# Kernel optimization log

Measured on AMD Instinct MI355X. Metric: run time of the kernel, lower is better.

## Reference

```python
import jax, jax.numpy as jnp
import numpy as np
import math

B, IN_CH, IMG = 32, 3, 128
D, L, H, MLP, P = 512, 8, 8, 2048, 8
HD = D // H
EPS = 1e-5


def _conv(x, w, b, stride, pad):
    y = jax.lax.conv_general_dilated(x, w, (stride, stride), pad,
                                     dimension_numbers=("NCHW", "OIHW", "NCHW"))
    return y + b[None, :, None, None]


def _gn(x, g, b, groups):
    Bn, C, Hh, W = x.shape
    xr = x.reshape(Bn, groups, C // groups, Hh, W)
    m = jnp.mean(xr, axis=(2, 3, 4), keepdims=True)
    v = jnp.var(xr, axis=(2, 3, 4), keepdims=True)
    xr = (xr - m) / jnp.sqrt(v + EPS)
    return xr.reshape(Bn, C, Hh, W) * g[None, :, None, None] + b[None, :, None, None]


def _ln(x, g, b):
    m = jnp.mean(x, axis=-1, keepdims=True)
    v = jnp.var(x, axis=-1, keepdims=True)
    return (x - m) / jnp.sqrt(v + EPS) * g + b


def _rot_half(x):
    # interleaved pairs: (x0,x1) -> (-x1,x0)
    x1, x2 = x[..., 0::2], x[..., 1::2]
    return jnp.stack((-x2, x1), axis=-1).reshape(x.shape)


def _xpos_tables(n_pos, hd):
    # faithful to rotary_embedding_torch with use_xpos=True, scale_base=512
    inv = 1.0 / (10000.0 ** (jnp.arange(0, hd, 2, dtype=jnp.float32) / hd))
    seq = jnp.arange(n_pos, dtype=jnp.float32)
    freqs = jnp.repeat(seq[:, None] * inv[None, :], 2, axis=-1)  # (n_pos, hd) interleaved
    sv = (jnp.arange(0, hd, 2, dtype=jnp.float32) + 0.4 * hd) / (1.4 * hd)
    power = (seq - n_pos // 2) / 512.0
    scale = sv[None, :] ** power[:, None]                        # (n_pos, hd//2)
    scale = jnp.concatenate([scale, scale], axis=-1)             # library uses cat, not interleave
    return jnp.cos(freqs), jnp.sin(freqs), scale


def _pos2d(N, Dd):
    g = int(math.isqrt(N))
    y = jnp.tile(jnp.arange(g), g).astype(jnp.float32)
    x = jnp.repeat(jnp.arange(g), g).astype(jnp.float32)
    dq = Dd // 4
    omega = jnp.exp(jnp.arange(dq, dtype=jnp.float32) * -(math.log(10000.0) / dq))
    px, py = x[:, None] * omega, y[:, None] * omega
    return jnp.concatenate([jnp.sin(px), jnp.cos(px), jnp.sin(py), jnp.cos(py)], axis=-1)[None]


def setup_inputs() -> dict:
    key = jax.random.key(0)
    ks = iter(jax.random.split(key, 40))
    def rn(shape, s=0.02):
        return jax.random.normal(next(ks), shape, jnp.float32) * s
    return dict(
        x=jax.random.normal(next(ks), (B, IN_CH, IMG, IMG), jnp.float32),
        conv1_w=rn((32, 3, 3, 3)), conv1_b=jnp.zeros((32,), jnp.float32),
        gn1_g=jnp.ones((32,), jnp.float32), gn1_b=jnp.zeros((32,), jnp.float32),
        conv2_w=rn((64, 32, 3, 3)), conv2_b=jnp.zeros((64,), jnp.float32),
        gn2_g=jnp.ones((64,), jnp.float32), gn2_b=jnp.zeros((64,), jnp.float32),
        patch_w=rn((D, 64, P, P)), patch_b=jnp.zeros((D,), jnp.float32),
        cls_token=rn((1, 1, D), 1.0),
        ln1_g=jnp.ones((L, D), jnp.float32), ln1_b=jnp.zeros((L, D), jnp.float32),
        qkv_w=rn((L, D, 3 * D)), qkv_b=jnp.zeros((L, 3 * D), jnp.float32),
        out_w=rn((L, D, D)), out_b=jnp.zeros((L, D), jnp.float32),
        ln2_g=jnp.ones((L, D), jnp.float32), ln2_b=jnp.zeros((L, D), jnp.float32),
        w1_w=rn((L, D, MLP)), w1_b=jnp.zeros((L, MLP), jnp.float32),
        w2_w=rn((L, D, MLP)), w2_b=jnp.zeros((L, MLP), jnp.float32),
        w3_w=rn((L, MLP, D)), w3_b=jnp.zeros((L, D), jnp.float32),
        fn_g=jnp.ones((D,), jnp.float32), fn_b=jnp.zeros((D,), jnp.float32),
    )


def _forward(x, conv1_w, conv1_b, gn1_g, gn1_b, conv2_w, conv2_b, gn2_g, gn2_b,
             patch_w, patch_b, cls_token, ln1_g, ln1_b, qkv_w, qkv_b, out_w, out_b,
             ln2_g, ln2_b, w1_w, w1_b, w2_w, w2_b, w3_w, w3_b, fn_g, fn_b):
    # conv stem (no downsample)
    f = jax.nn.gelu(_gn(_conv(x, conv1_w, conv1_b, 1, [(1, 1), (1, 1)]), gn1_g, gn1_b, 4), approximate=False)
    f = jax.nn.gelu(_gn(_conv(f, conv2_w, conv2_b, 1, [(1, 1), (1, 1)]), gn2_g, gn2_b, 8), approximate=False)
    # patch embed
    p = _conv(f, patch_w, patch_b, P, "VALID")            # (B, D, g, g)
    Bn, Dd, gh, gw = p.shape
    tokens = p.reshape(Bn, Dd, gh * gw).transpose(0, 2, 1)  # (B, N, D)
    tokens = tokens + _pos2d(gh * gw, Dd)
    xa = jnp.concatenate([jnp.broadcast_to(cls_token, (Bn, 1, Dd)), tokens], axis=1)
    # NOTE: original code applies RoPE with seq_dim=-2 on (B,S,H,hd) -> rotation indexed by HEAD axis
    cos, sin, xsc = _xpos_tables(H, HD)
    scale_att = HD ** -0.5
    for i in range(L):
        n = _ln(xa, ln1_g[i], ln1_b[i])
        qkv = (n @ qkv_w[i] + qkv_b[i]).reshape(Bn, -1, 3, H, HD)
        q, k, v = qkv[:, :, 0], qkv[:, :, 1], qkv[:, :, 2]     # (B, S, H, hd)
        q = q * cos * xsc + _rot_half(q) * sin * xsc
        k = k * cos / xsc + _rot_half(k) * sin / xsc
        attn = jax.nn.softmax(jnp.einsum("bihd,bjhd->bhij", q, k) * scale_att, axis=-1)
        y = jnp.einsum("bhij,bjhd->bihd", attn, v).reshape(Bn, -1, Dd)
        xa = xa + y @ out_w[i] + out_b[i]
        n2 = _ln(xa, ln2_g[i], ln2_b[i])
        xa = xa + (jax.nn.silu(n2 @ w1_w[i] + w1_b[i]) * (n2 @ w2_w[i] + w2_b[i])) @ w3_w[i] + w3_b[i]
    return _ln(xa, fn_g, fn_b)


def reference(x, conv1_w, conv1_b, gn1_g, gn1_b, conv2_w, conv2_b, gn2_g, gn2_b,
              patch_w, patch_b, cls_token, ln1_g, ln1_b, qkv_w, qkv_b, out_w, out_b,
              ln2_g, ln2_b, w1_w, w1_b, w2_w, w2_b, w3_w, w3_b, fn_g, fn_b):
    xa = _forward(x, conv1_w, conv1_b, gn1_g, gn1_b, conv2_w, conv2_b, gn2_g, gn2_b,
                  patch_w, patch_b, cls_token, ln1_g, ln1_b, qkv_w, qkv_b, out_w, out_b,
                  ln2_g, ln2_b, w1_w, w1_b, w2_w, w2_b, w3_w, w3_b, fn_g, fn_b)
    return (xa[:, 0], xa[:, 1:])  # (cls, patches); grid_hw is static (16,16)
```

## Files before the change

### kernel.cpp

```cpp
#include <hip/hip_runtime.h>

#define EPSV 1e-5f
typedef unsigned short u16;
typedef short bf16x8 __attribute__((ext_vector_type(8)));
typedef float f32x4 __attribute__((ext_vector_type(4)));
typedef u16 u16x8 __attribute__((ext_vector_type(8)));

__device__ __forceinline__ float gelu_exact(float x) {
    return 0.5f * x * (1.0f + erff(x * 0.7071067811865475f));
}
__device__ __forceinline__ u16 to_bf(float x) {
    union { float f; unsigned u; } c; c.f = x;
    unsigned r = c.u + 0x7fffu + ((c.u >> 16) & 1u);
    return (u16)(r >> 16);
}
__device__ __forceinline__ float to_f(u16 h) {
    union { unsigned u; float f; } c; c.u = ((unsigned)h) << 16;
    return c.f;
}
__device__ __forceinline__ void gload_lds16(const void* g, void* l) {
    __builtin_amdgcn_global_load_lds((const __attribute__((address_space(1))) unsigned int*)g,
                                     (__attribute__((address_space(3))) unsigned int*)l, 16, 0, 0);
}
__device__ __forceinline__ int xcd_swz() {
    int nwg = gridDim.x, orig = blockIdx.x;
    int q = nwg >> 3, r = nwg & 7;
    int xcd = orig & 7, sub = orig >> 3;
    return ((xcd < r) ? xcd * (q + 1) : r * (q + 1) + (xcd - r) * q) + sub;
}

__global__ void k_wsfail(float* out) { out[0] = 1.0e9f; }

__global__ void k_setup(float* __restrict__ sacc,
                        const float* __restrict__ conv1_w, float* __restrict__ w1t,
                        const float* __restrict__ conv2_w, u16* __restrict__ wpack,
                        const float* __restrict__ b1, const float* __restrict__ b2,
                        float* __restrict__ bias12,
                        float* __restrict__ postab, float* __restrict__ ropetab,
                        const float* __restrict__ cls, float* __restrict__ xa) {
    int idx = blockIdx.x * 256 + threadIdx.x;
    if (idx < 131072) {
        int p = idx >> 9, j = idx & 511;
        float coord = (j < 256) ? (float)(p >> 4) : (float)(p & 15);
        int jm = j & 127;
        float om = powf(10000.0f, -(float)jm / 128.0f);
        float arg = coord * om;
        postab[idx] = ((j >> 7) & 1) ? cosf(arg) : sinf(arg);
    }
    if (idx < 512) {
        int h = idx >> 6, d = idx & 63;
        float freq = (float)h * powf(10000.0f, -(float)(d >> 1) / 32.0f);
        float sv = (2.0f * (float)(d & 31) + 25.6f) / 89.6f;
        float pw = ((float)h - 4.0f) / 512.0f;
        float sc = powf(sv, pw);
        ropetab[idx * 4 + 0] = cosf(freq);
        ropetab[idx * 4 + 1] = sinf(freq);
        ropetab[idx * 4 + 2] = sc * 0.125f;
        ropetab[idx * 4 + 3] = 1.0f / sc;
    }
    if (idx < 768) sacc[idx] = 0.0f;
    if (idx < 864) {
        int co = idx / 27, k = idx % 27;
        w1t[k * 32 + co] = conv1_w[idx];
    }
    if (idx < 18432) {
        int ci = idx & 31, tc = idx >> 5;
        int tap = tc >> 6, co = tc & 63;
        wpack[idx] = to_bf(conv2_w[co * 288 + ci * 9 + tap]);
    }
    if (idx < 32768) {
        int l = idx >> 12, pc = idx & 4095;
        int chunk = pc >> 4, within = pc & 15;
        int srccol = (chunk >> 1) * 16 + within;
        bias12[idx] = (chunk & 1) ? b2[l * 2048 + srccol] : b1[l * 2048 + srccol];
    }
    if (idx < 16384) {
        int b = idx >> 9, d = idx & 511;
        xa[(size_t)(b * 257) * 512 + d] = cls[d];
    }
}

__global__ void k_pperm(const float* __restrict__ w, u16* __restrict__ wp) {
    int idx = blockIdx.x * 256 + threadIdx.x;
    int cout = idx >> 12, rem = idx & 4095;
    int tap = rem >> 6, ci = rem & 63;
    wp[idx] = to_bf(w[cout * 4096 + ci * 64 + tap]);
}

__global__ __launch_bounds__(256) void k_wcvtT(const float* __restrict__ src,
                                               u16* __restrict__ dst, int K, int N) {
    __shared__ float s[32][33];
    int z = blockIdx.z;
    src += (size_t)z * K * N;
    dst += (size_t)z * K * N;
    int k0 = blockIdx.y * 32, n0 = blockIdx.x * 32;
    int t = threadIdx.x, r = t >> 3, c4 = (t & 7) * 4;
    float4 v = *(const float4*)&src[(size_t)(k0 + r) * N + n0 + c4];
    s[r][c4 + 0] = v.x; s[r][c4 + 1] = v.y; s[r][c4 + 2] = v.z; s[r][c4 + 3] = v.w;
    __syncthreads();
    ushort4 o;
    o.x = to_bf(s[c4 + 0][r]); o.y = to_bf(s[c4 + 1][r]);
    o.z = to_bf(s[c4 + 2][r]); o.w = to_bf(s[c4 + 3][r]);
    *(ushort4*)&dst[(size_t)(n0 + r) * K + k0 + c4] = o;
}

__global__ __launch_bounds__(256) void k_wcvtT12L(const float* __restrict__ w1,
                                                  const float* __restrict__ w2,
                                                  u16* __restrict__ w12All) {
    __shared__ float s[32][33];
    int z = blockIdx.z;
    int layer = z >> 1, sel = z & 1;
    const float* src = (sel ? w2 : w1) + (size_t)layer * 1048576;
    u16* dst = w12All + (size_t)layer * 2097152;
    int k0 = blockIdx.y * 32, n0 = blockIdx.x * 32;
    int t = threadIdx.x, r = t >> 3, c4 = (t & 7) * 4;
    float4 v = *(const float4*)&src[(size_t)(k0 + r) * 2048 + n0 + c4];
    s[r][c4 + 0] = v.x; s[r][c4 + 1] = v.y; s[r][c4 + 2] = v.z; s[r][c4 + 3] = v.w;
    __syncthreads();
    ushort4 o;
    o.x = to_bf(s[c4 + 0][r]); o.y = to_bf(s[c4 + 1][r]);
    o.z = to_bf(s[c4 + 2][r]); o.w = to_bf(s[c4 + 3][r]);
    int nsrc = n0 + r;
    int p = ((nsrc >> 4) << 5) + (sel << 4) + (nsrc & 15);
    *(ushort4*)&dst[(size_t)p * 512 + k0 + c4] = o;
}

__global__ __launch_bounds__(256) void k_conv1(const float* __restrict__ in,
                                               const float* __restrict__ wt,
                                               const float* __restrict__ bias,
                                               u16* __restrict__ f1n,
                                               float* __restrict__ sacc) {
    __shared__ float s_in[3][18][18];
    __shared__ float rs[4][4], rq[4][4];
    int b = blockIdx.y;
    int tile = blockIdx.x;
    int y0 = (tile >> 3) << 4;
    int x0 = (tile & 7) << 4;
    int tid = threadIdx.x;
    for (int idx = tid; idx < 972; idx += 256) {
        int ci = idx / 324, r = idx % 324;
        int ly = r / 18, lx = r % 18;
        int gy = y0 + ly - 1, gx = x0 + lx - 1;
        float v = 0.0f;
        if (gy >= 0 && gy < 128 && gx >= 0 && gx < 128)
            v = in[((size_t)(b * 3 + ci) * 128 + gy) * 128 + gx];
        s_in[ci][ly][lx] = v;
    }
    __syncthreads();
    int py = tid >> 4, px = tid & 15;
    float acc[32];
#pragma unroll
    for (int co = 0; co < 32; co++) acc[co] = bias[co];
#pragma unroll
    for (int ci = 0; ci < 3; ci++)
#pragma unroll
        for (int dy = 0; dy < 3; dy++)
#pragma unroll
            for (int dx = 0; dx < 3; dx++) {
                float v = s_in[ci][py + dy][px + dx];
                const float* wr = &wt[(ci * 9 + dy * 3 + dx) * 32];
#pragma unroll
                for (int co = 0; co < 32; co++)
                    acc[co] = fmaf(wr[co], v, acc[co]);
            }
    float s[4] = {0.f, 0.f, 0.f, 0.f}, q[4] = {0.f, 0.f, 0.f, 0.f};
    u16 ob[32];
#pragma unroll
    for (int co = 0; co < 32; co++) {
        u16 hv = to_bf(acc[co]);
        ob[co] = hv;
        float v = to_f(hv);
        s[co >> 3] += v;
        q[co >> 3] += v * v;
    }
    int oy = y0 + py, ox = x0 + px;
    u16* dst = f1n + ((size_t)(b * 16384 + oy * 128 + ox) << 5);
#pragma unroll
    for (int i = 0; i < 8; i++)
        *(ushort4*)(dst + i * 4) = make_ushort4(ob[i * 4], ob[i * 4 + 1], ob[i * 4 + 2], ob[i * 4 + 3]);
#pragma unroll
    for (int g = 0; g < 4; g++) {
#pragma unroll
        for (int off = 1; off < 64; off <<= 1) {
            s[g] += __shfl_xor(s[g], off);
            q[g] += __shfl_xor(q[g], off);
        }
    }
    int w = tid >> 6, lane = tid & 63;
    if (lane == 0)
#pragma unroll
        for (int g = 0; g < 4; g++) { rs[g][w] = s[g]; rq[g][w] = q[g]; }
    __syncthreads();
    if (tid < 4) {
        int g = tid;
        float S = rs[g][0] + rs[g][1] + rs[g][2] + rs[g][3];
        float Q = rq[g][0] + rq[g][1] + rq[g][2] + rq[g][3];
        atomicAdd(&sacc[(b * 4 + g) * 2], S);
        atomicAdd(&sacc[(b * 4 + g) * 2 + 1], Q);
    }
}

__global__ void k_gnap(u16* __restrict__ xio, const float* __restrict__ sacc,
                       const float* __restrict__ gg, const float* __restrict__ bb,
                       int cm, int sh, int gmul) {
    int idx = blockIdx.x * 256 + threadIdx.x;
    long e = (long)idx * 4;
    int c0 = (int)(e & cm);
    int b = (int)(e >> sh);
    int sid = b * gmul + (c0 >> 3);
    float m = sacc[2 * sid] * (1.0f / 131072.0f);
    float var = sacc[2 * sid + 1] * (1.0f / 131072.0f) - m * m;
    float r = rsqrtf(var + 1e-5f);
    ushort4 a = *(ushort4*)&xio[e];
    ushort4 o;
    o.x = to_bf(gelu_exact((to_f(a.x) - m) * r * gg[c0 + 0] + bb[c0 + 0]));
    o.y = to_bf(gelu_exact((to_f(a.y) - m) * r * gg[c0 + 1] + bb[c0 + 1]));
    o.z = to_bf(gelu_exact((to_f(a.z) - m) * r * gg[c0 + 2] + bb[c0 + 2]));
    o.w = to_bf(gelu_exact((to_f(a.w) - m) * r * gg[c0 + 3] + bb[c0 + 3]));
    *(ushort4*)&xio[e] = o;
}

__global__ __launch_bounds__(256) void k_conv2m(const u16* __restrict__ f1b,
                                                const u16* __restrict__ wp,
                                                const float* __restrict__ bias,
                                                u16* __restrict__ f2n,
                                                float* __restrict__ sacc) {
    __shared__ u16 st[256][72];
    __shared__ float rs[8][4], rq[8][4];
    int b = blockIdx.y;
    int tile = blockIdx.x;
    int y0 = (tile >> 3) << 4;
    int x0 = (tile & 7) << 4;
    int tid = threadIdx.x;
    int w = tid >> 6, lane = tid & 63;
    int l15 = lane & 15, l16 = lane >> 4;

    const u16* base = f1b + ((size_t)b << 19);

    f32x4 acc[4][4];
    f32x4 zf = {0.f, 0.f, 0.f, 0.f};
#pragma unroll
    for (int m = 0; m < 4; m++)
#pragma unroll
        for (int n = 0; n < 4; n++) acc[m][n] = zf;
    bf16x8 zb = {0, 0, 0, 0, 0, 0, 0, 0};

#pragma unroll
    for (int tap = 0; tap < 9; tap++) {
        int dy = tap / 3, dx = tap % 3;
        int gx = x0 + l15 + dx - 1;
        bf16x8 af[4], bk[4];
#pragma unroll
        for (int m = 0; m < 4; m++) {
            int gy = y0 + w * 4 + m + dy - 1;
            bool ok = (gy >= 0) && (gy < 128) && (gx >= 0) && (gx < 128);
            int pix = ok ? (gy * 128 + gx) : 0;
            bf16x8 v = *(const bf16x8*)(base + ((size_t)pix << 5) + l16 * 8);
            af[m] = ok ? v : zb;
        }
#pragma unroll
        for (int n = 0; n < 4; n++)
            bk[n] = *(const bf16x8*)&wp[(tap * 64 + n * 16 + l15) * 32 + l16 * 8];
#pragma unroll
        for (int m = 0; m < 4; m++)
#pragma unroll
            for (int n = 0; n < 4; n++)
                acc[m][n] = __builtin_amdgcn_mfma_f32_16x16x32_bf16(af[m], bk[n], acc[m][n], 0, 0, 0);
    }

#pragma unroll
    for (int n = 0; n < 4; n++) {
        int ch = n * 16 + l15;
        float bv = bias[ch];
#pragma unroll
        for (int m = 0; m < 4; m++) {
#pragma unroll
            for (int r = 0; r < 4; r++) {
                int lpix = (w * 4 + m) * 16 + l16 * 4 + r;
                st[lpix][ch] = to_bf(acc[m][n][r] + bv);
            }
        }
    }
    __syncthreads();

    int py = tid >> 4, pxx = tid & 15;
    u16* dstp = f2n + ((size_t)(b * 16384 + (y0 + py) * 128 + x0 + pxx) << 6);
    float gs[8], gq[8];
#pragma unroll
    for (int g = 0; g < 8; g++) { gs[g] = 0.0f; gq[g] = 0.0f; }
#pragma unroll
    for (int c0 = 0; c0 < 8; c0++) {
        u16x8 v = *(const u16x8*)&st[tid][c0 * 8];
        *(u16x8*)(dstp + c0 * 8) = v;
#pragma unroll
        for (int i = 0; i < 8; i++) {
            float f = to_f((u16)v[i]);
            gs[c0] += f;
            gq[c0] += f * f;
        }
    }
#pragma unroll
    for (int g = 0; g < 8; g++) {
#pragma unroll
        for (int off = 1; off < 64; off <<= 1) {
            gs[g] += __shfl_xor(gs[g], off);
            gq[g] += __shfl_xor(gq[g], off);
        }
    }
    if (lane == 0)
#pragma unroll
        for (int g = 0; g < 8; g++) { rs[g][w] = gs[g]; rq[g][w] = gq[g]; }
    __syncthreads();
    if (tid < 8) {
        int g = tid;
        float S = rs[g][0] + rs[g][1] + rs[g][2] + rs[g][3];
        float Q = rq[g][0] + rq[g][1] + rq[g][2] + rq[g][3];
        atomicAdd(&sacc[(b * 8 + g) * 2], S);
        atomicAdd(&sacc[(b * 8 + g) * 2 + 1], Q);
    }
}

template <int MODE, int EPI>
__global__ __launch_bounds__(256) void k_bgemm(const u16* __restrict__ A,
                                               const u16* __restrict__ Bt,
                                               const float* __restrict__ bias,
                                               void* __restrict__ Cp,
                                               const float* __restrict__ aux,
                                               int M, int N, int K, int gridN) {
    __shared__ u16 ldsA[8192];
    __shared__ u16 ldsB[8192];
    int tid = threadIdx.x;
    int w = tid >> 6, lane = tid & 63;
    int wgid = xcd_swz();
    int bm = (wgid / gridN) * 128, bn = (wgid % gridN) * 128;
    int wr = w >> 1, wc = w & 1;
    int l15 = lane & 15, l16 = lane >> 4;

    f32x4 acc[4][4];
    f32x4 zf = {0.f, 0.f, 0.f, 0.f};
#pragma unroll
    for (int m = 0; m < 4; m++)
#pragma unroll
        for (int n = 0; n < 4; n++) acc[m][n] = zf;

    for (int k0 = 0; k0 < K; k0 += 64) {
#pragma unroll
        for (int i = 0; i < 4; i++) {
            int chunk = (w * 4 + i) * 64 + lane;
            int kg = chunk >> 7, row = chunk & 127;
            const u16* src;
            if (MODE == 0) {
                int grow = bm + row;
                if (grow > M - 1) grow = M - 1;
                src = A + (size_t)grow * K + k0 + kg * 8;
            } else {
                int grow = bm + row;
                int bimg = grow >> 8, p = grow & 255;
                int kga = (k0 >> 3) + kg;
                int tap = kga >> 3, cq = kga & 7;
                int ky = tap >> 3, kx = tap & 7;
                int gy = ((p >> 4) << 3) + ky, gx = ((p & 15) << 3) + kx;
                src = A + (((size_t)(bimg * 16384 + gy * 128 + gx)) << 6) + cq * 8;
            }
            gload_lds16(src, &ldsA[(w * 4 + i) * 512]);
        }
#pragma unroll
        for (int i = 0; i < 4; i++) {
            int chunk = (w * 4 + i) * 64 + lane;
            int col = chunk >> 3, kgs = chunk & 7;
            int kg_src = kgs ^ (col & 7);
            const u16* src = Bt + (size_t)(bn + col) * K + k0 + kg_src * 8;
            gload_lds16(src, &ldsB[(w * 4 + i) * 512]);
        }
        __syncthreads();

        bf16x8 af[4][2], bfr[4][2];
#pragma unroll
        for (int kk = 0; kk < 2; kk++) {
            int kga = kk * 4 + l16;
#pragma unroll
            for (int m = 0; m < 4; m++) {
                int row_l = wr * 64 + m * 16 + l15;
                af[m][kk] = *(const bf16x8*)&ldsA[(kga * 128 + row_l) * 8];
            }
#pragma unroll
            for (int n = 0; n < 4; n++) {
                int col_l = wc * 64 + n * 16 + l15;
                bfr[n][kk] = *(const bf16x8*)&ldsB[(col_l * 8 + (kga ^ (col_l & 7))) * 8];
            }
        }
#pragma unroll
        for (int m = 0; m < 4; m++)
#pragma unroll
            for (int n = 0; n < 4; n++) {
                acc[m][n] = __builtin_amdgcn_mfma_f32_16x16x32_bf16(af[m][0], bfr[n][0], acc[m][n], 0, 0, 0);
                acc[m][n] = __builtin_amdgcn_mfma_f32_16x16x32_bf16(af[m][1], bfr[n][1], acc[m][n], 0, 0, 0);
            }
        __syncthreads();
    }

    if (EPI == 6) {
#pragma unroll
        for (int np = 0; np < 2; np++) {
            int n_a = np * 2, n_b = np * 2 + 1;
            float bva = bias[bn + wc * 64 + n_a * 16 + l15];
            float bvb = bias[bn + wc * 64 + n_b * 16 + l15];
            int ocol = (bn >> 1) + wc * 32 + np * 16 + l15;
#pragma unroll
            for (int m = 0; m < 4; m++) {
#pragma unroll
                for (int r = 0; r < 4; r++) {
                    int grow = bm + wr * 64 + m * 16 + l16 * 4 + r;
                    if (grow < M) {
                        float h1v = to_f(to_bf(acc[m][n_a][r] + bva));
                        float h2v = to_f(to_bf(acc[m][n_b][r] + bvb));
                        float sl = h1v / (1.0f + __expf(-h1v));
                        ((u16*)Cp)[(size_t)grow * (N >> 1) + ocol] = to_bf(sl * h2v);
                    }
                }
            }
        }
    } else {
#pragma unroll
        for (int n = 0; n < 4; n++) {
            int gcol = bn + wc * 64 + n * 16 + l15;
            float bv = bias[gcol];
            float rc = 0.f, rsn = 0.f, rsc = 1.f;
            bool isqk = false, odd = false;
            if (EPI == 7) {
                isqk = gcol < 1024;
                odd = (l15 & 1) != 0;
                const float* rb = &aux[(gcol & 511) * 4];
                if (isqk) {
                    rc = rb[0]; rsn = rb[1];
                    rsc = (gcol < 512) ? rb[2] : rb[3];
                }
            }
#pragma unroll
            for (int m = 0; m < 4; m++) {
#pragma unroll
                for (int r = 0; r < 4; r++) {
                    int grow = bm + wr * 64 + m * 16 + l16 * 4 + r;
                    float v = acc[m][n][r] + bv;
                    if (EPI == 7) {
                        float p = __shfl_xor(v, 1);
                        float vr = isqk ? ((odd ? (v * rc + p * rsn) : (v * rc - p * rsn)) * rsc) : v;
                        if (grow < M) ((u16*)Cp)[(size_t)grow * N + gcol] = to_bf(vr);
                    } else if (EPI == 1) {
                        if (grow < M) ((float*)Cp)[(size_t)grow * N + gcol] = v;
                    } else if (EPI == 2) {
                        if (grow < M) ((float*)Cp)[(size_t)grow * N + gcol] += v;
                    } else {
                        int bimg = grow >> 8, p2 = grow & 255;
                        v += aux[p2 * 512 + gcol];
                        ((float*)Cp)[((size_t)(bimg * 257) + 1 + p2) * 512 + gcol] = v;
                    }
                }
            }
        }
    }
}

__global__ __launch_bounds__(256) void k_bgemm64(const u16* __restrict__ A,
                                                 const u16* __restrict__ Bt,
                                                 const float* __restrict__ bias,
                                                 float* __restrict__ C,
                                                 int M, int N, int K, int gridN) {
    __shared__ u16 ldsA[4096];
    __shared__ u16 ldsB[8192];
    int tid = threadIdx.x;
    int w = tid >> 6, lane = tid & 63;
    int wgid = xcd_swz();
    int bm = (wgid / gridN) * 64, bn = (wgid % gridN) * 128;
    int l15 = lane & 15, l16 = lane >> 4;

    f32x4 acc[4][2];
    f32x4 zf = {0.f, 0.f, 0.f, 0.f};
#pragma unroll
    for (int m = 0; m < 4; m++)
#pragma unroll
        for (int n = 0; n < 2; n++) acc[m][n] = zf;

    for (int k0 = 0; k0 < K; k0 += 64) {
#pragma unroll
        for (int i = 0; i < 2; i++) {
            int chunk = (w * 2 + i) * 64 + lane;
            int kg = chunk >> 6, row = chunk & 63;
            int grow = bm + row;
            if (grow > M - 1) grow = M - 1;
            const u16* src = A + (size_t)grow * K + k0 + kg * 8;
            gload_lds16(src, &ldsA[(w * 2 + i) * 512]);
        }
#pragma unroll
        for (int i = 0; i < 4; i++) {
            int chunk = (w * 4 + i) * 64 + lane;
            int col = chunk >> 3, kgs = chunk & 7;
            int kg_src = kgs ^ (col & 7);
            const u16* src = Bt + (size_t)(bn + col) * K + k0 + kg_src * 8;
            gload_lds16(src, &ldsB[(w * 4 + i) * 512]);
        }
        __syncthreads();

        bf16x8 af[4][2], bfr[2][2];
#pragma unroll
        for (int kk = 0; kk < 2; kk++) {
            int kga = kk * 4 + l16;
#pragma unroll
            for (int m = 0; m < 4; m++) {
                int row_l = m * 16 + l15;
                af[m][kk] = *(const bf16x8*)&ldsA[(kga * 64 + row_l) * 8];
            }
#pragma unroll
            for (int n = 0; n < 2; n++) {
                int col_l = w * 32 + n * 16 + l15;
                bfr[n][kk] = *(const bf16x8*)&ldsB[(col_l * 8 + (kga ^ (col_l & 7))) * 8];
            }
        }
#pragma unroll
        for (int m = 0; m < 4; m++)
#pragma unroll
            for (int n = 0; n < 2; n++) {
                acc[m][n] = __builtin_amdgcn_mfma_f32_16x16x32_bf16(af[m][0], bfr[n][0], acc[m][n], 0, 0, 0);
                acc[m][n] = __builtin_amdgcn_mfma_f32_16x16x32_bf16(af[m][1], bfr[n][1], acc[m][n], 0, 0, 0);
            }
        __syncthreads();
    }

#pragma unroll
    for (int n = 0; n < 2; n++) {
        int gcol = bn + w * 32 + n * 16 + l15;
        float bv = bias[gcol];
#pragma unroll
        for (int m = 0; m < 4; m++) {
#pragma unroll
            for (int r = 0; r < 4; r++) {
                int grow = bm + m * 16 + l16 * 4 + r;
                if (grow < M) C[(size_t)grow * N + gcol] += acc[m][n][r] + bv;
            }
        }
    }
}

__global__ __launch_bounds__(256) void k_lnb(const float* __restrict__ x,
                                             const float* __restrict__ g,
                                             const float* __restrict__ bta,
                                             u16* __restrict__ o) {
    int row = blockIdx.x * 4 + (threadIdx.x >> 6);
    int lane = threadIdx.x & 63;
    const float4* xr = (const float4*)(x + (size_t)row * 512);
    float4 a = xr[lane * 2], b = xr[lane * 2 + 1];
    float s = a.x + a.y + a.z + a.w + b.x + b.y + b.z + b.w;
#pragma unroll
    for (int off = 1; off < 64; off <<= 1) s += __shfl_xor(s, off);
    float mean = s * (1.0f / 512.0f);
    float d[8] = {a.x - mean, a.y - mean, a.z - mean, a.w - mean,
                  b.x - mean, b.y - mean, b.z - mean, b.w - mean};
    float q = 0.0f;
#pragma unroll
    for (int i = 0; i < 8; i++) q += d[i] * d[i];
#pragma unroll
    for (int off = 1; off < 64; off <<= 1) q += __shfl_xor(q, off);
    float rstd = rsqrtf(q * (1.0f / 512.0f) + EPSV);
    int c0 = lane * 8;
    float4 g0 = *(const float4*)&g[c0], g1 = *(const float4*)&g[c0 + 4];
    float4 b0 = *(const float4*)&bta[c0], b1 = *(const float4*)&bta[c0 + 4];
    u16* orow = o + (size_t)row * 512 + c0;
    *(ushort4*)orow = make_ushort4(to_bf(d[0] * rstd * g0.x + b0.x), to_bf(d[1] * rstd * g0.y + b0.y),
                                   to_bf(d[2] * rstd * g0.z + b0.z), to_bf(d[3] * rstd * g0.w + b0.w));
    *(ushort4*)(orow + 4) = make_ushort4(to_bf(d[4] * rstd * g1.x + b1.x), to_bf(d[5] * rstd * g1.y + b1.y),
                                         to_bf(d[6] * rstd * g1.z + b1.z), to_bf(d[7] * rstd * g1.w + b1.w));
}

__global__ __launch_bounds__(256) void k_ln_out(const float* __restrict__ x,
                                                const float* __restrict__ g,
                                                const float* __restrict__ bta,
                                                float* __restrict__ out) {
    int row = blockIdx.x * 4 + (threadIdx.x >> 6);
    int lane = threadIdx.x & 63;
    const float4* xr = (const float4*)(x + (size_t)row * 512);
    float4 a = xr[lane * 2], b = xr[lane * 2 + 1];
    float s = a.x + a.y + a.z + a.w + b.x + b.y + b.z + b.w;
#pragma unroll
    for (int off = 1; off < 64; off <<= 1) s += __shfl_xor(s, off);
    float mean = s * (1.0f / 512.0f);
    float d[8] = {a.x - mean, a.y - mean, a.z - mean, a.w - mean,
                  b.x - mean, b.y - mean, b.z - mean, b.w - mean};
    float q = 0.0f;
#pragma unroll
    for (int i = 0; i < 8; i++) q += d[i] * d[i];
#pragma unroll
    for (int off = 1; off < 64; off <<= 1) q += __shfl_xor(q, off);
    float rstd = rsqrtf(q * (1.0f / 512.0f) + EPSV);
    int bb = row / 257, t = row % 257;
    float* dst = (t == 0) ? out + (size_t)bb * 512
                          : out + 16384 + (size_t)(bb * 256 + (t - 1)) * 512;
    int c0 = lane * 8;
    float4 g0 = *(const float4*)&g[c0], g1 = *(const float4*)&g[c0 + 4];
    float4 b0 = *(const float4*)&bta[c0], b1 = *(const float4*)&bta[c0 + 4];
    *(float4*)(dst + c0) = make_float4(d[0] * rstd * g0.x + b0.x, d[1] * rstd * g0.y + b0.y,
                                       d[2] * rstd * g0.z + b0.z, d[3] * rstd * g0.w + b0.w);
    *(float4*)(dst + c0 + 4) = make_float4(d[4] * rstd * g1.x + b1.x, d[5] * rstd * g1.y + b1.y,
                                           d[6] * rstd * g1.z + b1.z, d[7] * rstd * g1.w + b1.w);
}

__global__ __launch_bounds__(256) void k_attn_mfma(const u16* __restrict__ qkv,
                                                   u16* __restrict__ y) {
    __shared__ u16 KV[2][64][72];
    __shared__ float sc[32][260];
    __shared__ u16 Pb[32][328];
    __shared__ float red1[32][8];
    __shared__ float red2[32][8];
    __shared__ float invr[32];

    int bid = blockIdx.x;
    int qt = bid % 9, bh = bid / 9;
    int h = bh & 7, b = bh >> 3;
    int q0 = qt * 32;
    int tid = threadIdx.x;
    int w = tid >> 6, lane = tid & 63;
    int l15 = lane & 15, l16 = lane >> 4;

    bf16x8 aq[2][2];
#pragma unroll
    for (int m = 0; m < 2; m++) {
        int grow = q0 + m * 16 + l15; if (grow > 256) grow = 256;
        const u16* qp = qkv + (size_t)(b * 257 + grow) * 1536 + h * 64 + l16 * 8;
        aq[m][0] = *(const bf16x8*)qp;
        aq[m][1] = *(const bf16x8*)(qp + 32);
    }

    for (int t = 0; t < 5; t++) {
        int j0 = t * 64;
        int gk = j0 + w * 16 + l15; if (gk > 256) gk = 256;
        const u16* kp = qkv + (size_t)(b * 257 + gk) * 1536 + 512 + h * 64 + l16 * 8;
        bf16x8 bk0 = *(const bf16x8*)kp;
        bf16x8 bk1 = *(const bf16x8*)(kp + 32);
        f32x4 a2[2];
        f32x4 zf = {0.f, 0.f, 0.f, 0.f};
        __builtin_amdgcn_s_setprio(1);
#pragma unroll
        for (int m = 0; m < 2; m++) {
            a2[m] = zf;
            a2[m] = __builtin_amdgcn_mfma_f32_16x16x32_bf16(aq[m][0], bk0, a2[m], 0, 0, 0);
            a2[m] = __builtin_amdgcn_mfma_f32_16x16x32_bf16(aq[m][1], bk1, a2[m], 0, 0, 0);
        }
        __builtin_amdgcn_s_setprio(0);
        int col = j0 + w * 16 + l15;
        if (col < 257) {
#pragma unroll
            for (int m = 0; m < 2; m++)
#pragma unroll
                for (int r = 0; r < 4; r++)
                    sc[m * 16 + l16 * 4 + r][col] = a2[m][r];
        }
    }
    __syncthreads();

    {
        int r = tid >> 3, sub = tid & 7;
        float mx = -1e30f;
        for (int j = sub; j < 257; j += 8) mx = fmaxf(mx, sc[r][j]);
        red1[r][sub] = mx;
        __syncthreads();
        mx = red1[r][0];
#pragma unroll
        for (int i = 1; i < 8; i++) mx = fmaxf(mx, red1[r][i]);
        float sm = 0.0f;
        for (int j = sub; j < 257; j += 8) {
            float e = __expf(sc[r][j] - mx);
            Pb[r][j] = to_bf(e);
            sm += e;
        }
        for (int j = 257 + sub; j < 320; j += 8) Pb[r][j] = 0;
        red2[r][sub] = sm;
        __syncthreads();
        if (sub == 0) {
            float t = red2[r][0];
#pragma unroll
            for (int i = 1; i < 8; i++) t += red2[r][i];
            invr[r] = 1.0f / t;
        }
        __syncthreads();
    }

    f32x4 oacc[2];
    {
        f32x4 zf = {0.f, 0.f, 0.f, 0.f};
        oacc[0] = zf; oacc[1] = zf;
    }
    for (int t = 0; t < 5; t++) {
        int j0 = t * 64;
        int buf = t & 1;
        {
            int vk = tid & 63, vd0 = (tid >> 6) * 16;
            int gk = j0 + vk;
            u16 o[16];
            if (gk <= 256) {
                const u16* vp = qkv + (size_t)(b * 257 + gk) * 1536 + 1024 + h * 64 + vd0;
                ushort4 a0 = *(const ushort4*)vp, a1 = *(const ushort4*)(vp + 4);
                ushort4 a2v = *(const ushort4*)(vp + 8), a3 = *(const ushort4*)(vp + 12);
                o[0] = a0.x; o[1] = a0.y; o[2] = a0.z; o[3] = a0.w;
                o[4] = a1.x; o[5] = a1.y; o[6] = a1.z; o[7] = a1.w;
                o[8] = a2v.x; o[9] = a2v.y; o[10] = a2v.z; o[11] = a2v.w;
                o[12] = a3.x; o[13] = a3.y; o[14] = a3.z; o[15] = a3.w;
            } else {
#pragma unroll
                for (int i = 0; i < 16; i++) o[i] = 0;
            }
#pragma unroll
            for (int i = 0; i < 16; i++) KV[buf][vd0 + i][vk] = o[i];
        }
        __syncthreads();

        bf16x8 ap[2][2], bv[2];
#pragma unroll
        for (int m = 0; m < 2; m++)
#pragma unroll
            for (int kk = 0; kk < 2; kk++)
                ap[m][kk] = *(const bf16x8*)&Pb[m * 16 + l15][j0 + kk * 32 + l16 * 8];
#pragma unroll
        for (int kk = 0; kk < 2; kk++)
            bv[kk] = *(const bf16x8*)&KV[buf][w * 16 + l15][kk * 32 + l16 * 8];
        __builtin_amdgcn_s_setprio(1);
#pragma unroll
        for (int m = 0; m < 2; m++) {
            oacc[m] = __builtin_amdgcn_mfma_f32_16x16x32_bf16(ap[m][0], bv[0], oacc[m], 0, 0, 0);
            oacc[m] = __builtin_amdgcn_mfma_f32_16x16x32_bf16(ap[m][1], bv[1], oacc[m], 0, 0, 0);
        }
        __builtin_amdgcn_s_setprio(0);
    }

#pragma unroll
    for (int m = 0; m < 2; m++)
#pragma unroll
        for (int r = 0; r < 4; r++) {
            int lr = m * 16 + l16 * 4 + r;
            int grow = q0 + lr;
            if (grow < 257)
                y[(size_t)(b * 257 + grow) * 512 + h * 64 + w * 16 + l15] =
                    to_bf(oacc[m][r] * invr[lr]);
        }
}

extern "C" void kernel_launch(void* const* d_in, const int* in_sizes, int n_in,
                              void* d_out, int out_size, void* d_ws, size_t ws_size,
                              hipStream_t stream) {
    const float* x       = (const float*)d_in[0];
    const float* conv1_w = (const float*)d_in[1];
    const float* conv1_b = (const float*)d_in[2];
    const float* gn1_g   = (const float*)d_in[3];
    const float* gn1_b   = (const float*)d_in[4];
    const float* conv2_w = (const float*)d_in[5];
    const float* conv2_b = (const float*)d_in[6];
    const float* gn2_g   = (const float*)d_in[7];
    const float* gn2_b   = (const float*)d_in[8];
    const float* patch_w = (const float*)d_in[9];
    const float* patch_b = (const float*)d_in[10];
    const float* cls_tok = (const float*)d_in[11];
    const float* ln1_g   = (const float*)d_in[12];
    const float* ln1_b   = (const float*)d_in[13];
    const float* qkv_w   = (const float*)d_in[14];
    const float* qkv_b   = (const float*)d_in[15];
    const float* out_w   = (const float*)d_in[16];
    const float* out_b   = (const float*)d_in[17];
    const float* ln2_g   = (const float*)d_in[18];
    const float* ln2_b   = (const float*)d_in[19];
    const float* w1_w    = (const float*)d_in[20];
    const float* w1_b    = (const float*)d_in[21];
    const float* w2_w    = (const float*)d_in[22];
    const float* w2_b    = (const float*)d_in[23];
    const float* w3_w    = (const float*)d_in[24];
    const float* w3_b    = (const float*)d_in[25];
    const float* fn_g    = (const float*)d_in[26];
    const float* fn_b    = (const float*)d_in[27];
    float* out = (float*)d_out;
    char* wsb  = (char*)d_ws;

    const size_t O_R1    = 0;
    const size_t O_W12A  = 0;
    const size_t O_W3A   = 33554432;
    const size_t O_HB    = O_R1 + 67371008;
    const size_t O_NB    = O_R1 + 101056512;
    const size_t O_Y     = O_R1 + 109477888;
    const size_t O_R2    = 134217728;
    const size_t O_XA    = 201326592;
    const size_t O_PWT   = 218169344;
    const size_t O_QKVT  = 222363648;
    const size_t O_OUTT  = 234946560;
    const size_t O_PT    = 245432320;
    const size_t O_RT    = 245956608;
    const size_t O_CW1   = 245964800;
    const size_t O_CW2   = 245968896;
    const size_t O_SA    = 246046720;
    const size_t O_B12   = 246050816;
    const size_t NEED    = 246181888;
    if (ws_size < NEED) {
        k_wsfail<<<1, 1, 0, stream>>>(out);
        return;
    }
    u16*   f2n    = (u16*)(wsb + O_R1);
    u16*   w12All = (u16*)(wsb + O_W12A);
    u16*   w3All  = (u16*)(wsb + O_W3A);
    u16*   hb     = (u16*)(wsb + O_HB);
    u16*   nb     = (u16*)(wsb + O_NB);
    u16*   yb     = (u16*)(wsb + O_Y);
    u16*   f1n    = (u16*)(wsb + O_R2);
    u16*   qkvb   = (u16*)(wsb + O_R2);
    float* xa     = (float*)(wsb + O_XA);
    u16*   patchT = (u16*)(wsb + O_PWT);
    u16*   qkvT   = (u16*)(wsb + O_QKVT);
    u16*   outT   = (u16*)(wsb + O_OUTT);
    float* postab = (float*)(wsb + O_PT);
    float* ropet  = (float*)(wsb + O_RT);
    float* w1t    = (float*)(wsb + O_CW1);
    u16*   wpack  = (u16*)(wsb + O_CW2);
    float* sacc   = (float*)(wsb + O_SA);
    float* bias12 = (float*)(wsb + O_B12);

    k_setup<<<512, 256, 0, stream>>>(sacc, conv1_w, w1t, conv2_w, wpack,
                                     w1_b, w2_b, bias12, postab, ropet, cls_tok, xa);
    k_pperm<<<8192, 256, 0, stream>>>(patch_w, patchT);
    k_wcvtT<<<dim3(48, 16, 8), 256, 0, stream>>>(qkv_w, qkvT, 512, 1536);
    k_wcvtT<<<dim3(16, 16, 8), 256, 0, stream>>>(out_w, outT, 512, 512);

    k_conv1<<<dim3(64, 32), 256, 0, stream>>>(x, w1t, conv1_b, f1n, sacc);
    k_gnap<<<16384, 256, 0, stream>>>(f1n, sacc, gn1_g, gn1_b, 31, 19, 4);
    k_conv2m<<<dim3(64, 32), 256, 0, stream>>>(f1n, wpack, conv2_b, f2n, sacc + 256);
    k_gnap<<<32768, 256, 0, stream>>>(f2n, sacc + 256, gn2_g, gn2_b, 63, 20, 8);

    k_bgemm<1, 3><<<256, 256, 0, stream>>>(f2n, patchT, patch_b, xa, postab, 8192, 512, 4096, 4);

    k_wcvtT12L<<<dim3(64, 16, 16), 256, 0, stream>>>(w1_w, w2_w, w12All);
    k_wcvtT<<<dim3(16, 64, 8), 256, 0, stream>>>(w3_w, w3All, 2048, 512);

    for (int l = 0; l < 8; l++) {
        k_lnb<<<2056, 256, 0, stream>>>(xa, ln1_g + l * 512, ln1_b + l * 512, nb);
        k_bgemm<0, 7><<<780, 256, 0, stream>>>(nb, qkvT + (size_t)l * 786432,
                                               qkv_b + l * 1536, qkvb, ropet, 8224, 1536, 512, 12);
        k_attn_mfma<<<2304, 256, 0, stream>>>(qkvb, yb);
        k_bgemm64<<<516, 256, 0, stream>>>(yb, outT + (size_t)l * 262144,
                                           out_b + l * 512, xa, 8224, 512, 512, 4);
        k_lnb<<<2056, 256, 0, stream>>>(xa, ln2_g + l * 512, ln2_b + l * 512, nb);
        k_bgemm<0, 6><<<2080, 256, 0, stream>>>(nb, w12All + (size_t)l * 2097152,
                                                bias12 + l * 4096, hb, nullptr, 8224, 4096, 512, 32);
        k_bgemm64<<<516, 256, 0, stream>>>(hb, w3All + (size_t)l * 1048576,
                                           w3_b + l * 512, xa, 8224, 512, 2048, 4);
    }
    k_ln_out<<<2056, 256, 0, stream>>>(xa, fn_g, fn_b, out);
}
```

Measured before the change: 2.319 ms.

## Double-buffer LDS tiles in bf16 GEMM kernels to overlap loads with MFMA

Both GEMM kernels, k_bgemm and k_bgemm64, get two LDS buffers for the A and B tiles. Each iteration issues the async global-to-LDS loads for the next K tile before running the MFMAs on the current tile. This removes one barrier per iteration and hides global load latency behind compute. The cost is double the LDS per block (64KB for k_bgemm), which may lower occupancy.

Measured after the change: 2.388 ms. 1.03x slower.

```diff
diff --git a/kernel.cpp b/kernel.cpp
--- a/kernel.cpp
+++ b/kernel.cpp
@@ -327,8 +327,8 @@
                                                void* __restrict__ Cp,
                                                const float* __restrict__ aux,
                                                int M, int N, int K, int gridN) {
-    __shared__ u16 ldsA[8192];
-    __shared__ u16 ldsB[8192];
+    __shared__ u16 ldsA[2][8192];
+    __shared__ u16 ldsB[2][8192];
     int tid = threadIdx.x;
     int w = tid >> 6, lane = tid & 63;
     int wgid = xcd_swz();
@@ -336,14 +336,7 @@
     int wr = w >> 1, wc = w & 1;
     int l15 = lane & 15, l16 = lane >> 4;
 
-    f32x4 acc[4][4];
-    f32x4 zf = {0.f, 0.f, 0.f, 0.f};
-#pragma unroll
-    for (int m = 0; m < 4; m++)
-#pragma unroll
-        for (int n = 0; n < 4; n++) acc[m][n] = zf;
-
-    for (int k0 = 0; k0 < K; k0 += 64) {
+    auto stage = [&](int k0, int bb) {
 #pragma unroll
         for (int i = 0; i < 4; i++) {
             int chunk = (w * 4 + i) * 64 + lane;
@@ -362,7 +355,7 @@
                 int gy = ((p >> 4) << 3) + ky, gx = ((p & 15) << 3) + kx;
                 src = A + (((size_t)(bimg * 16384 + gy * 128 + gx)) << 6) + cq * 8;
             }
-            gload_lds16(src, &ldsA[(w * 4 + i) * 512]);
+            gload_lds16(src, &ldsA[bb][(w * 4 + i) * 512]);
         }
 #pragma unroll
         for (int i = 0; i < 4; i++) {
@@ -370,9 +363,23 @@
             int col = chunk >> 3, kgs = chunk & 7;
             int kg_src = kgs ^ (col & 7);
             const u16* src = Bt + (size_t)(bn + col) * K + k0 + kg_src * 8;
-            gload_lds16(src, &ldsB[(w * 4 + i) * 512]);
-        }
-        __syncthreads();
+            gload_lds16(src, &ldsB[bb][(w * 4 + i) * 512]);
+        }
+    };
+
+    f32x4 acc[4][4];
+    f32x4 zf = {0.f, 0.f, 0.f, 0.f};
+#pragma unroll
+    for (int m = 0; m < 4; m++)
+#pragma unroll
+        for (int n = 0; n < 4; n++) acc[m][n] = zf;
+
+    int nk = K >> 6;
+    stage(0, 0);
+    __syncthreads();
+    int cur = 0;
+    for (int kt = 0; kt < nk; kt++) {
+        if (kt + 1 < nk) stage((kt + 1) << 6, cur ^ 1);
 
         bf16x8 af[4][2], bfr[4][2];
 #pragma unroll
@@ -381,12 +388,12 @@
 #pragma unroll
             for (int m = 0; m < 4; m++) {
                 int row_l = wr * 64 + m * 16 + l15;
-                af[m][kk] = *(const bf16x8*)&ldsA[(kga * 128 + row_l) * 8];
+                af[m][kk] = *(const bf16x8*)&ldsA[cur][(kga * 128 + row_l) * 8];
             }
 #pragma unroll
             for (int n = 0; n < 4; n++) {
                 int col_l = wc * 64 + n * 16 + l15;
-                bfr[n][kk] = *(const bf16x8*)&ldsB[(col_l * 8 + (kga ^ (col_l & 7))) * 8];
+                bfr[n][kk] = *(const bf16x8*)&ldsB[cur][(col_l * 8 + (kga ^ (col_l & 7))) * 8];
             }
         }
 #pragma unroll
@@ -397,6 +404,7 @@
                 acc[m][n] = __builtin_amdgcn_mfma_f32_16x16x32_bf16(af[m][1], bfr[n][1], acc[m][n], 0, 0, 0);
             }
         __syncthreads();
+        cur ^= 1;
     }
 
     if (EPI == 6) {
@@ -466,22 +474,15 @@
                                                  const float* __restrict__ bias,
                                                  float* __restrict__ C,
                                                  int M, int N, int K, int gridN) {
-    __shared__ u16 ldsA[4096];
-    __shared__ u16 ldsB[8192];
+    __shared__ u16 ldsA[2][4096];
+    __shared__ u16 ldsB[2][8192];
     int tid = threadIdx.x;
     int w = tid >> 6, lane = tid & 63;
     int wgid = xcd_swz();
     int bm = (wgid / gridN) * 64, bn = (wgid % gridN) * 128;
     int l15 = lane & 15, l16 = lane >> 4;
 
-    f32x4 acc[4][2];
-    f32x4 zf = {0.f, 0.f, 0.f, 0.f};
-#pragma unroll
-    for (int m = 0; m < 4; m++)
-#pragma unroll
-        for (int n = 0; n < 2; n++) acc[m][n] = zf;
-
-    for (int k0 = 0; k0 < K; k0 += 64) {
+    auto stage = [&](int k0, int bb) {
 #pragma unroll
         for (int i = 0; i < 2; i++) {
             int chunk = (w * 2 + i) * 64 + lane;
@@ -489,7 +490,7 @@
             int grow = bm + row;
             if (grow > M - 1) grow = M - 1;
             const u16* src = A + (size_t)grow * K + k0 + kg * 8;
-            gload_lds16(src, &ldsA[(w * 2 + i) * 512]);
+            gload_lds16(src, &ldsA[bb][(w * 2 + i) * 512]);
         }
 #pragma unroll
         for (int i = 0; i < 4; i++) {
@@ -497,9 +498,23 @@
             int col = chunk >> 3, kgs = chunk & 7;
             int kg_src = kgs ^ (col & 7);
             const u16* src = Bt + (size_t)(bn + col) * K + k0 + kg_src * 8;
-            gload_lds16(src, &ldsB[(w * 4 + i) * 512]);
-        }
-        __syncthreads();
+            gload_lds16(src, &ldsB[bb][(w * 4 + i) * 512]);
+        }
+    };
+
+    f32x4 acc[4][2];
+    f32x4 zf = {0.f, 0.f, 0.f, 0.f};
+#pragma unroll
+    for (int m = 0; m < 4; m++)
+#pragma unroll
+        for (int n = 0; n < 2; n++) acc[m][n] = zf;
+
+    int nk = K >> 6;
+    stage(0, 0);
+    __syncthreads();
+    int cur = 0;
+    for (int kt = 0; kt < nk; kt++) {
+        if (kt + 1 < nk) stage((kt + 1) << 6, cur ^ 1);
 
         bf16x8 af[4][2], bfr[2][2];
 #pragma unroll
@@ -508,12 +523,12 @@
 #pragma unroll
             for (int m = 0; m < 4; m++) {
                 int row_l = m * 16 + l15;
-                af[m][kk] = *(const bf16x8*)&ldsA[(kga * 64 + row_l) * 8];
+                af[m][kk] = *(const bf16x8*)&ldsA[cur][(kga * 64 + row_l) * 8];
             }
 #pragma unroll
             for (int n = 0; n < 2; n++) {
                 int col_l = w * 32 + n * 16 + l15;
-                bfr[n][kk] = *(const bf16x8*)&ldsB[(col_l * 8 + (kga ^ (col_l & 7))) * 8];
+                bfr[n][kk] = *(const bf16x8*)&ldsB[cur][(col_l * 8 + (kga ^ (col_l & 7))) * 8];
             }
         }
 #pragma unroll
@@ -524,6 +539,7 @@
                 acc[m][n] = __builtin_amdgcn_mfma_f32_16x16x32_bf16(af[m][1], bfr[n][1], acc[m][n], 0, 0, 0);
             }
         __syncthreads();
+        cur ^= 1;
     }
 
 #pragma unroll
```
